# Optimization experiments

Measured on AMD Instinct MI355X. Metric: run time of the kernel, lower is better.

Reference implementation:

```python
import jax, jax.numpy as jnp
import numpy as np

H = 16          # num_heads
MAX_SCALE_MUL = float(np.log(100.0))
EPS = 1e-12     # F.normalize eps


def setup_inputs() -> dict:
    key = jax.random.key(0)
    ks = jax.random.split(key, 8)
    B, L, C = 8, 1024, 1024
    x = jax.random.normal(ks[0], (B, L, C), dtype=jnp.float32)
    attn_bias = jax.random.normal(ks[1], (1, H, L, L), dtype=jnp.float32) * 0.1
    w_qkv = jax.random.normal(ks[2], (3 * C, C), dtype=jnp.float32) * (C ** -0.5)
    q_bias = jnp.zeros((C,), dtype=jnp.float32)
    v_bias = jnp.zeros((C,), dtype=jnp.float32)
    scale_mul = jnp.full((1, H, 1, 1), np.log(4.0), dtype=jnp.float32)
    w_proj = jax.random.normal(ks[3], (C, C), dtype=jnp.float32) * (C ** -0.5)
    b_proj = jnp.zeros((C,), dtype=jnp.float32)
    return dict(x=x, attn_bias=attn_bias, w_qkv=w_qkv, q_bias=q_bias,
                v_bias=v_bias, scale_mul=scale_mul, w_proj=w_proj, b_proj=b_proj)


def _l2norm(t):
    # matches F.normalize(dim=-1): t / max(||t||_2, eps)
    n = jnp.sqrt(jnp.sum(t * t, axis=-1, keepdims=True))
    return t / jnp.maximum(n, EPS)


def reference(x, attn_bias, w_qkv, q_bias, v_bias, scale_mul, w_proj, b_proj):
    B, L, C = x.shape
    D = C // H
    bias = jnp.concatenate([q_bias, jnp.zeros_like(q_bias), v_bias])
    qkv = x @ w_qkv.T + bias                      # [B,L,3C]
    qkv = qkv.reshape(B, L, 3, H, D).transpose(2, 0, 3, 1, 4)  # [3,B,H,L,D]
    q, k, v = qkv[0], qkv[1], qkv[2]
    sm = jnp.exp(jnp.minimum(scale_mul, MAX_SCALE_MUL))        # [1,H,1,1]
    q = _l2norm(q) * sm
    k = _l2norm(k)
    attn = jnp.einsum('bhld,bhmd->bhlm', q, k) + attn_bias     # scale == 1
    attn = jax.nn.softmax(attn, axis=-1)
    out = jnp.einsum('bhlm,bhmd->bhld', attn, v)               # [B,H,L,D]
    out = out.transpose(0, 2, 1, 3).reshape(B, L, C)
    return out @ w_proj.T + b_proj
```

## Files before the change

### kernel.cpp

```cpp
#include <hip/hip_runtime.h>


#define LN100 4.6051701859880914f

typedef __attribute__((ext_vector_type(8))) short short8;
typedef __attribute__((ext_vector_type(4))) float f32x4;

#define MFMA_BF16(a, b, c) __builtin_amdgcn_mfma_f32_16x16x32_bf16(a, b, c, 0, 0, 0)

__device__ __forceinline__ unsigned short f2bf(float f) {
  unsigned u = __float_as_uint(f);
  u += 0x7fffu + ((u >> 16) & 1u);
  return (unsigned short)(u >> 16);
}
__device__ __forceinline__ float bf2f(unsigned short h) {
  return __uint_as_float(((unsigned)h) << 16);
}

__device__ __forceinline__ float bias_sel0(const float* qb, const float* vb, int col) {
  if (col < 1024) return qb[col];
  if (col < 2048) return 0.0f;
  return vb[col - 2048];
}

#define G2L16(gp, lp) __builtin_amdgcn_global_load_lds( \
    (const __attribute__((address_space(1))) void*)(gp), \
    (__attribute__((address_space(3))) void*)(lp), 16, 0, 0)

__global__ __launch_bounds__(256)
void split_f32_bf16(const float* __restrict__ in, unsigned short* __restrict__ hi,
                    unsigned short* __restrict__ lo, int n4)
{
  int i = blockIdx.x * blockDim.x + threadIdx.x;
  if (i >= n4) return;
  float4 v = ((const float4*)in)[i];
  ushort4 h, l;
  h.x = f2bf(v.x); l.x = f2bf(v.x - bf2f(h.x));
  h.y = f2bf(v.y); l.y = f2bf(v.y - bf2f(h.y));
  h.z = f2bf(v.z); l.z = f2bf(v.z - bf2f(h.z));
  h.w = f2bf(v.w); l.w = f2bf(v.w - bf2f(h.w));
  ((ushort4*)hi)[i] = h;
  ((ushort4*)lo)[i] = l;
}

template <int MODE>
__global__ __launch_bounds__(256)
void gemm_nt_split(const unsigned short* __restrict__ Ah, const unsigned short* __restrict__ Al,
                   const unsigned short* __restrict__ Wh, const unsigned short* __restrict__ Wl,
                   const float* __restrict__ b0, const float* __restrict__ b1,
                   float* __restrict__ C, int M, int N, int K)
{
  __shared__ unsigned short sA[128 * 64];
  __shared__ unsigned short sW[128 * 64];

  const int tid  = threadIdx.x;
  const int lane = tid & 63;
  const int l15  = lane & 15, lg = lane >> 4;
  const int w    = tid >> 6;
  const int wr   = (w >> 1) << 6;
  const int wc   = (w & 1) << 6;
  const int m0   = blockIdx.y << 7;
  const int n0   = blockIdx.x << 7;

  f32x4 acc[4][4];
  #pragma unroll
  for (int i = 0; i < 4; ++i)
    #pragma unroll
    for (int j = 0; j < 4; ++j)
      acc[i][j] = (f32x4){0.f, 0.f, 0.f, 0.f};

  for (int k0 = 0; k0 < K; k0 += 32) {
    __syncthreads();
    #pragma unroll
    for (int u = 0; u < 4; ++u) {
      int idx = (u << 8) + tid;
      int row = idx >> 3;
      int c   = idx & 7;
      int s   = c ^ (row & 7);
      size_t rbA = (size_t)(m0 + row) * K + k0;
      size_t rbW = (size_t)(n0 + row) * K + k0;
      const unsigned short* srcA = (s < 4) ? (Ah + rbA + (s << 3))
                                           : (Al + rbA + ((s - 4) << 3));
      const unsigned short* srcW = (s < 4) ? (Wh + rbW + (s << 3))
                                           : (Wl + rbW + ((s - 4) << 3));
      G2L16(srcA, sA + (idx << 3));
      G2L16(srcW, sW + (idx << 3));
    }
    __syncthreads();

    short8 ah[4], al[4];
    #pragma unroll
    for (int i = 0; i < 4; ++i) {
      int row = wr + (i << 4) + l15;
      ah[i] = *(const short8*)(sA + (row << 6) + ((lg       ^ (row & 7)) << 3));
      al[i] = *(const short8*)(sA + (row << 6) + (((4 + lg) ^ (row & 7)) << 3));
    }
    #pragma unroll
    for (int j = 0; j < 4; ++j) {
      int row = wc + (j << 4) + l15;
      short8 wh = *(const short8*)(sW + (row << 6) + ((lg       ^ (row & 7)) << 3));
      short8 wl = *(const short8*)(sW + (row << 6) + (((4 + lg) ^ (row & 7)) << 3));
      #pragma unroll
      for (int i = 0; i < 4; ++i) {
        acc[i][j] = MFMA_BF16(ah[i], wh, acc[i][j]);
        acc[i][j] = MFMA_BF16(ah[i], wl, acc[i][j]);
        acc[i][j] = MFMA_BF16(al[i], wh, acc[i][j]);
      }
    }
  }

  #pragma unroll
  for (int j = 0; j < 4; ++j) {
    int col = n0 + wc + (j << 4) + l15;
    float bb = (MODE == 0) ? bias_sel0(b0, b1, col) : b0[col];
    #pragma unroll
    for (int i = 0; i < 4; ++i) {
      int rbase = m0 + wr + (i << 4) + (lg << 2);
      #pragma unroll
      for (int r = 0; r < 4; ++r)
        C[(size_t)(rbase + r) * N + col] = acc[i][j][r] + bb;
    }
  }
}

__global__ __launch_bounds__(256)
void qk_norm_split(const float* __restrict__ qkv, const float* __restrict__ scale_mul,
                   unsigned short* __restrict__ qk_h, unsigned short* __restrict__ qk_l)
{
  int wave = (blockIdx.x << 2) + (threadIdx.x >> 6);
  int lane = threadIdx.x & 63;
  int h  = wave & 15;
  int bl = wave >> 4;
  size_t base = (size_t)bl * 3072 + (h << 6) + lane;
  float q = qkv[base];
  float k = qkv[base + 1024];
  float sq = q * q, sk = k * k;
  #pragma unroll
  for (int off = 32; off; off >>= 1) {
    sq += __shfl_xor(sq, off);
    sk += __shfl_xor(sk, off);
  }
  float sm = __expf(fminf(scale_mul[h], LN100));
  q = q / fmaxf(sqrtf(sq), 1e-12f) * sm;
  k = k / fmaxf(sqrtf(sk), 1e-12f);
  size_t ob = (size_t)bl * 2048 + (h << 6) + lane;
  unsigned short qh = f2bf(q);
  qk_h[ob] = qh;          qk_l[ob] = f2bf(q - bf2f(qh));
  unsigned short kh = f2bf(k);
  qk_h[ob + 1024] = kh;   qk_l[ob + 1024] = f2bf(k - bf2f(kh));
}

__global__ __launch_bounds__(256)
void v_split_t(const float* __restrict__ qkv, unsigned short* __restrict__ vth,
               unsigned short* __restrict__ vtl)
{
  __shared__ unsigned short Th[64][136];
  __shared__ unsigned short Tl[64][136];
  const int tid = threadIdx.x;
  const int kc = blockIdx.x & 7;
  const int h  = (blockIdx.x >> 3) & 15;
  const int b  = blockIdx.x >> 7;
  const int kv0 = kc << 7;

  #pragma unroll
  for (int u = 0; u < 8; ++u) {
    int idx = (u << 8) + tid;
    int kv  = idx >> 4;
    int d4  = (idx & 15) << 2;
    float4 v = *(const float4*)(qkv + (size_t)((b << 10) + kv0 + kv) * 3072
                                    + 2048 + (h << 6) + d4);
    float e[4] = {v.x, v.y, v.z, v.w};
    #pragma unroll
    for (int j = 0; j < 4; ++j) {
      unsigned short hb = f2bf(e[j]);
      Th[d4 + j][kv] = hb;
      Tl[d4 + j][kv] = f2bf(e[j] - bf2f(hb));
    }
  }
  __syncthreads();

  const size_t ob = ((size_t)((b << 4) + h) << 6) * 1024;
  #pragma unroll
  for (int u = 0; u < 4; ++u) {
    int idx = (u << 8) + tid;
    int d  = idx >> 4;
    int cc = idx & 15;
    short8 hv = *(const short8*)(&Th[d][cc << 3]);
    short8 lv = *(const short8*)(&Tl[d][cc << 3]);
    size_t go = ob + (size_t)d * 1024 + kv0 + (cc << 3);
    *(short8*)(vth + go) = hv;
    *(short8*)(vtl + go) = lv;
  }
}

__global__ __launch_bounds__(256)
void attn_mfma(const unsigned short* __restrict__ qk_h, const unsigned short* __restrict__ qk_l,
               const unsigned short* __restrict__ vth, const unsigned short* __restrict__ vtl,
               const float* __restrict__ bias,
               unsigned short* __restrict__ oh, unsigned short* __restrict__ ol)
{
  __shared__ unsigned short sKh[4096], sKl[4096];
  __shared__ unsigned short sVh[4096], sVl[4096];
  __shared__ unsigned short sPh[4096], sPl[4096];

  const int tid  = threadIdx.x;
  const int lane = tid & 63;
  const int l15  = lane & 15, lg = lane >> 4;
  const int w    = tid >> 6;
  const int qt = blockIdx.x & 15;
  const int h  = (blockIdx.x >> 4) & 15;
  const int b  = blockIdx.x >> 8;
  const int q0 = qt << 6;

  short8 qh[2], qlo[2];
  {
    size_t rb = ((size_t)((b << 10) + q0 + (w << 4) + l15)) * 2048 + (h << 6) + (lg << 3);
    qh[0]  = *(const short8*)(qk_h + rb);
    qh[1]  = *(const short8*)(qk_h + rb + 32);
    qlo[0] = *(const short8*)(qk_l + rb);
    qlo[1] = *(const short8*)(qk_l + rb + 32);
  }

  f32x4 ao[4];
  #pragma unroll
  for (int j = 0; j < 4; ++j) ao[j] = (f32x4){0.f, 0.f, 0.f, 0.f};
  float mr[4], lr[4];
  #pragma unroll
  for (int r = 0; r < 4; ++r) { mr[r] = -3.0e38f; lr[r] = 0.0f; }

  const unsigned short* kh_base = qk_h + 1024 + (h << 6);
  const unsigned short* kl_base = qk_l + 1024 + (h << 6);
  const size_t vbase = ((size_t)((b << 4) + h)) * 65536;

  for (int kv0 = 0; kv0 < 1024; kv0 += 64) {
    __syncthreads();
    #pragma unroll
    for (int u = 0; u < 2; ++u) {
      int idx = (u << 8) + tid;
      int r = idx >> 3, c = idx & 7;
      int s = c ^ (r & 7);
      size_t krow = (size_t)((b << 10) + kv0 + r) * 2048 + (s << 3);
      size_t vrow = vbase + (size_t)r * 1024 + kv0 + (s << 3);
      G2L16(kh_base + krow, sKh + (idx << 3));
      G2L16(kl_base + krow, sKl + (idx << 3));
      G2L16(vth + vrow,     sVh + (idx << 3));
      G2L16(vtl + vrow,     sVl + (idx << 3));
    }
    __syncthreads();

    f32x4 sv[4];
    #pragma unroll
    for (int j = 0; j < 4; ++j) {
      f32x4 a = (f32x4){0.f, 0.f, 0.f, 0.f};
      #pragma unroll
      for (int ks = 0; ks < 2; ++ks) {
        int row = (j << 4) + l15;
        int c   = (lg + (ks << 2)) ^ (row & 7);
        short8 kh = *(const short8*)(sKh + (row << 6) + (c << 3));
        short8 kl = *(const short8*)(sKl + (row << 6) + (c << 3));
        a = MFMA_BF16(qh[ks], kh, a);
        a = MFMA_BF16(qh[ks], kl, a);
        a = MFMA_BF16(qlo[ks], kh, a);
      }
      sv[j] = a;
    }

    float p[4][4], alpha[4];
    #pragma unroll
    for (int r = 0; r < 4; ++r) {
      int qrow = q0 + (w << 4) + (lg << 2) + r;
      const float* bp = bias + ((size_t)h << 20) + (size_t)qrow * 1024 + kv0 + l15;
      float s0 = sv[0][r] + bp[0];
      float s1 = sv[1][r] + bp[16];
      float s2 = sv[2][r] + bp[32];
      float s3 = sv[3][r] + bp[48];
      float mx = fmaxf(fmaxf(s0, s1), fmaxf(s2, s3));
      #pragma unroll
      for (int o = 1; o < 16; o <<= 1) mx = fmaxf(mx, __shfl_xor(mx, o));
      float mn = fmaxf(mr[r], mx);
      alpha[r] = __expf(mr[r] - mn);
      p[r][0] = __expf(s0 - mn); p[r][1] = __expf(s1 - mn);
      p[r][2] = __expf(s2 - mn); p[r][3] = __expf(s3 - mn);
      float rs = p[r][0] + p[r][1] + p[r][2] + p[r][3];
      #pragma unroll
      for (int o = 1; o < 16; o <<= 1) rs += __shfl_xor(rs, o);
      lr[r] = lr[r] * alpha[r] + rs;
      mr[r] = mn;
    }

    #pragma unroll
    for (int jd = 0; jd < 4; ++jd)
      #pragma unroll
      for (int r = 0; r < 4; ++r)
        ao[jd][r] *= alpha[r];

    #pragma unroll
    for (int r = 0; r < 4; ++r) {
      int q2 = (w << 4) + (lg << 2) + r;
      #pragma unroll
      for (int j = 0; j < 4; ++j) {
        unsigned short hb = f2bf(p[r][j]);
        unsigned short lb = f2bf(p[r][j] - bf2f(hb));
        int c = ((j << 1) + (l15 >> 3)) ^ (q2 & 7);
        int e = (q2 << 6) + (c << 3) + (l15 & 7);
        sPh[e] = hb;
        sPl[e] = lb;
      }
    }

    #pragma unroll
    for (int ks = 0; ks < 2; ++ks) {
      int prow = (w << 4) + l15;
      int pc   = (lg + (ks << 2)) ^ (prow & 7);
      short8 ph = *(const short8*)(sPh + (prow << 6) + (pc << 3));
      short8 pl = *(const short8*)(sPl + (prow << 6) + (pc << 3));
      #pragma unroll
      for (int jd = 0; jd < 4; ++jd) {
        int vrow = (jd << 4) + l15;
        int vc   = (lg + (ks << 2)) ^ (vrow & 7);
        short8 vh = *(const short8*)(sVh + (vrow << 6) + (vc << 3));
        short8 vl = *(const short8*)(sVl + (vrow << 6) + (vc << 3));
        ao[jd] = MFMA_BF16(ph, vh, ao[jd]);
        ao[jd] = MFMA_BF16(ph, vl, ao[jd]);
        ao[jd] = MFMA_BF16(pl, vh, ao[jd]);
      }
    }
  }

  #pragma unroll
  for (int r = 0; r < 4; ++r) {
    float inv = 1.0f / lr[r];
    size_t orow = ((size_t)((b << 10) + q0 + (w << 4) + (lg << 2) + r)) * 1024
                + (h << 6) + l15;
    #pragma unroll
    for (int jd = 0; jd < 4; ++jd) {
      float v = ao[jd][r] * inv;
      unsigned short hb = f2bf(v);
      oh[orow + (jd << 4)] = hb;
      ol[orow + (jd << 4)] = f2bf(v - bf2f(hb));
    }
  }
}

template <int MODE>
__global__ __launch_bounds__(256)
void gemm_nt(const float* __restrict__ A, const float* __restrict__ Bw,
             const float* __restrict__ b0, const float* __restrict__ b1,
             float* __restrict__ C, int M, int N, int K)
{
  __shared__ float As[32][132];
  __shared__ float Bs[32][132];
  const int tid = threadIdx.x;
  const int tx = tid & 15, ty = tid >> 4;
  const int m0 = blockIdx.y << 7;
  const int n0 = blockIdx.x << 7;

  float acc[8][8];
  #pragma unroll
  for (int i = 0; i < 8; ++i)
    #pragma unroll
    for (int j = 0; j < 8; ++j) acc[i][j] = 0.0f;

  for (int k0 = 0; k0 < K; k0 += 32) {
    #pragma unroll
    for (int u = 0; u < 4; ++u) {
      int f   = tid + (u << 8);
      int row = f >> 3;
      int kk  = (f & 7) << 2;
      float4 av = *(const float4*)(A  + (size_t)(m0 + row) * K + k0 + kk);
      As[kk + 0][row] = av.x; As[kk + 1][row] = av.y;
      As[kk + 2][row] = av.z; As[kk + 3][row] = av.w;
      float4 bv = *(const float4*)(Bw + (size_t)(n0 + row) * K + k0 + kk);
      Bs[kk + 0][row] = bv.x; Bs[kk + 1][row] = bv.y;
      Bs[kk + 2][row] = bv.z; Bs[kk + 3][row] = bv.w;
    }
    __syncthreads();
    #pragma unroll
    for (int kk = 0; kk < 32; ++kk) {
      float a[8], b[8];
      *(float4*)(a)     = *(const float4*)(&As[kk][(ty << 3)]);
      *(float4*)(a + 4) = *(const float4*)(&As[kk][(ty << 3) + 4]);
      *(float4*)(b)     = *(const float4*)(&Bs[kk][(tx << 3)]);
      *(float4*)(b + 4) = *(const float4*)(&Bs[kk][(tx << 3) + 4]);
      #pragma unroll
      for (int i = 0; i < 8; ++i)
        #pragma unroll
        for (int j = 0; j < 8; ++j)
          acc[i][j] = fmaf(a[i], b[j], acc[i][j]);
    }
    __syncthreads();
  }

  #pragma unroll
  for (int i = 0; i < 8; ++i) {
    int row = m0 + (ty << 3) + i;
    #pragma unroll
    for (int j4 = 0; j4 < 2; ++j4) {
      int col = n0 + (tx << 3) + (j4 << 2);
      float4 r;
      float bb[4];
      #pragma unroll
      for (int j = 0; j < 4; ++j)
        bb[j] = (MODE == 0) ? bias_sel0(b0, b1, col + j) : b0[col + j];
      r.x = acc[i][j4 * 4 + 0] + bb[0];
      r.y = acc[i][j4 * 4 + 1] + bb[1];
      r.z = acc[i][j4 * 4 + 2] + bb[2];
      r.w = acc[i][j4 * 4 + 3] + bb[3];
      *(float4*)(C + (size_t)row * N + col) = r;
    }
  }
}

__global__ __launch_bounds__(256)
void qk_norm(float* __restrict__ qkv, const float* __restrict__ scale_mul)
{
  int wave = (blockIdx.x << 2) + (threadIdx.x >> 6);
  int lane = threadIdx.x & 63;
  int h  = wave & 15;
  int bl = wave >> 4;
  size_t base = (size_t)bl * 3072 + (h << 6) + lane;
  float q = qkv[base];
  float k = qkv[base + 1024];
  float sq = q * q, sk = k * k;
  #pragma unroll
  for (int off = 32; off; off >>= 1) {
    sq += __shfl_xor(sq, off);
    sk += __shfl_xor(sk, off);
  }
  float sm = __expf(fminf(scale_mul[h], LN100));
  q = q / fmaxf(sqrtf(sq), 1e-12f) * sm;
  k = k / fmaxf(sqrtf(sk), 1e-12f);
  qkv[base]        = q;
  qkv[base + 1024] = k;
}

#define SW(r, c4) ((((c4) ^ ((r) >> 2)) & 15) << 2)

template <int OUTMODE>
__global__ __launch_bounds__(256)
void attn_fwd(const float* __restrict__ qkv, const float* __restrict__ bias,
              float* __restrict__ aout,
              unsigned short* __restrict__ ah, unsigned short* __restrict__ al)
{
  __shared__ float Qs[64][64];
  __shared__ float Ks[64][64];
  __shared__ float Vs[64][64];
  __shared__ float Ps[64][64];

  const int tid = threadIdx.x;
  const int tx = tid & 15, ty = tid >> 4;
  const int qt = blockIdx.x & 15;
  const int h  = (blockIdx.x >> 4) & 15;
  const int b  = blockIdx.x >> 8;
  const int q0 = qt << 6;

  #pragma unroll
  for (int u = 0; u < 4; ++u) {
    int f = tid + (u << 8);
    int r = f >> 4, c4 = f & 15;
    float4 v = *(const float4*)(qkv + (size_t)(b * 1024 + q0 + r) * 3072 + (h << 6) + (c4 << 2));
    *(float4*)(&Qs[r][SW(r, c4)]) = v;
  }

  float o[4][4];
  float mr[4], lr[4];
  #pragma unroll
  for (int i = 0; i < 4; ++i) {
    mr[i] = -3.0e38f; lr[i] = 0.0f;
    #pragma unroll
    for (int j = 0; j < 4; ++j) o[i][j] = 0.0f;
  }

  for (int kv0 = 0; kv0 < 1024; kv0 += 64) {
    __syncthreads();
    #pragma unroll
    for (int u = 0; u < 4; ++u) {
      int f = tid + (u << 8);
      int r = f >> 4, c4 = f & 15;
      size_t gb = (size_t)(b * 1024 + kv0 + r) * 3072 + (h << 6) + (c4 << 2);
      *(float4*)(&Ks[r][SW(r, c4)]) = *(const float4*)(qkv + gb + 1024);
      *(float4*)(&Vs[r][SW(r, c4)]) = *(const float4*)(qkv + gb + 2048);
    }
    __syncthreads();

    float s[4][4];
    #pragma unroll
    for (int i = 0; i < 4; ++i)
      #pragma unroll
      for (int j = 0; j < 4; ++j) s[i][j] = 0.0f;

    #pragma unroll 4
    for (int d4 = 0; d4 < 16; ++d4) {
      float4 qv[4], kv[4];
      #pragma unroll
      for (int i = 0; i < 4; ++i)
        qv[i] = *(const float4*)(&Qs[(ty << 2) + i][SW((ty << 2) + i, d4)]);
      #pragma unroll
      for (int j = 0; j < 4; ++j)
        kv[j] = *(const float4*)(&Ks[(tx << 2) + j][SW((tx << 2) + j, d4)]);
      #pragma unroll
      for (int i = 0; i < 4; ++i)
        #pragma unroll
        for (int j = 0; j < 4; ++j)
          s[i][j] += qv[i].x * kv[j].x + qv[i].y * kv[j].y +
                     qv[i].z * kv[j].z + qv[i].w * kv[j].w;
    }

    float p[4][4];
    #pragma unroll
    for (int i = 0; i < 4; ++i) {
      float4 bv = *(const float4*)(bias + (size_t)((h << 10) + q0 + (ty << 2) + i) * 1024
                                        + kv0 + (tx << 2));
      s[i][0] += bv.x; s[i][1] += bv.y; s[i][2] += bv.z; s[i][3] += bv.w;
      float mx = fmaxf(fmaxf(s[i][0], s[i][1]), fmaxf(s[i][2], s[i][3]));
      #pragma unroll
      for (int off = 1; off < 16; off <<= 1) mx = fmaxf(mx, __shfl_xor(mx, off));
      float mn = fmaxf(mr[i], mx);
      float alp = __expf(mr[i] - mn);
      float rs = 0.0f;
      #pragma unroll
      for (int j = 0; j < 4; ++j) { p[i][j] = __expf(s[i][j] - mn); rs += p[i][j]; }
      #pragma unroll
      for (int off = 1; off < 16; off <<= 1) rs += __shfl_xor(rs, off);
      lr[i] = lr[i] * alp + rs;
      mr[i] = mn;
      #pragma unroll
      for (int j = 0; j < 4; ++j) o[i][j] *= alp;
    }

    #pragma unroll
    for (int jj = 0; jj < 4; ++jj)
      #pragma unroll
      for (int i = 0; i < 4; ++i)
        Ps[(tx << 2) + jj][SW((tx << 2) + jj, ty) + i] = p[i][jj];
    __syncthreads();

    #pragma unroll 8
    for (int j = 0; j < 64; ++j) {
      float4 pv = *(const float4*)(&Ps[j][SW(j, ty)]);
      float4 vv = *(const float4*)(&Vs[j][SW(j, tx)]);
      o[0][0] += pv.x * vv.x; o[0][1] += pv.x * vv.y; o[0][2] += pv.x * vv.z; o[0][3] += pv.x * vv.w;
      o[1][0] += pv.y * vv.x; o[1][1] += pv.y * vv.y; o[1][2] += pv.y * vv.z; o[1][3] += pv.y * vv.w;
      o[2][0] += pv.z * vv.x; o[2][1] += pv.z * vv.y; o[2][2] += pv.z * vv.z; o[2][3] += pv.z * vv.w;
      o[3][0] += pv.w * vv.x; o[3][1] += pv.w * vv.y; o[3][2] += pv.w * vv.z; o[3][3] += pv.w * vv.w;
    }
  }

  #pragma unroll
  for (int i = 0; i < 4; ++i) {
    float inv = 1.0f / lr[i];
    float v0 = o[i][0] * inv, v1 = o[i][1] * inv, v2 = o[i][2] * inv, v3 = o[i][3] * inv;
    if (OUTMODE == 0) {
      float4 r; r.x = v0; r.y = v1; r.z = v2; r.w = v3;
      *(float4*)(aout + (size_t)(b * 1024 + q0 + (ty << 2) + i) * 1024 + (h << 6) + (tx << 2)) = r;
    } else {
      ushort4 hh, ll;
      hh.x = f2bf(v0); ll.x = f2bf(v0 - bf2f(hh.x));
      hh.y = f2bf(v1); ll.y = f2bf(v1 - bf2f(hh.y));
      hh.z = f2bf(v2); ll.z = f2bf(v2 - bf2f(hh.z));
      hh.w = f2bf(v3); ll.w = f2bf(v3 - bf2f(hh.w));
      size_t idx = (size_t)(b * 1024 + q0 + (ty << 2) + i) * 256 + (h << 4) + tx;
      ((ushort4*)ah)[idx] = hh;
      ((ushort4*)al)[idx] = ll;
    }
  }
}

extern "C" void kernel_launch(void* const* d_in, const int* in_sizes, int n_in,
                              void* d_out, int out_size, void* d_ws, size_t ws_size,
                              hipStream_t stream) {
  const float* x         = (const float*)d_in[0];
  const float* attn_bias = (const float*)d_in[1];
  const float* w_qkv     = (const float*)d_in[2];
  const float* q_bias    = (const float*)d_in[3];
  const float* v_bias    = (const float*)d_in[4];
  const float* scale_mul = (const float*)d_in[5];
  const float* w_proj    = (const float*)d_in[6];
  const float* b_proj    = (const float*)d_in[7];
  float* out = (float*)d_out;

  const size_t MiB = 1024 * 1024;
  char* ws = (char*)d_ws;
  dim3 blk(256);

  if (ws_size >= 240 * MiB) {
    float*          qkv = (float*)ws;
    unsigned short* xh  = (unsigned short*)(ws + 96  * MiB);
    unsigned short* xl  = (unsigned short*)(ws + 112 * MiB);
    unsigned short* qkh = (unsigned short*)(ws + 128 * MiB);
    unsigned short* qkl = (unsigned short*)(ws + 160 * MiB);
    unsigned short* vth = (unsigned short*)(ws + 192 * MiB);
    unsigned short* vtl = (unsigned short*)(ws + 208 * MiB);
    unsigned short* wqh = (unsigned short*)(ws + 224 * MiB);
    unsigned short* wql = (unsigned short*)(ws + 230 * MiB);
    unsigned short* wph = (unsigned short*)(ws + 236 * MiB);
    unsigned short* wpl = (unsigned short*)(ws + 238 * MiB);

    split_f32_bf16<<<dim3(8192), blk, 0, stream>>>(x,      xh,  xl,  2097152);
    split_f32_bf16<<<dim3(3072), blk, 0, stream>>>(w_qkv,  wqh, wql, 786432);
    split_f32_bf16<<<dim3(1024), blk, 0, stream>>>(w_proj, wph, wpl, 262144);

    gemm_nt_split<0><<<dim3(24, 64), blk, 0, stream>>>(xh, xl, wqh, wql,
        q_bias, v_bias, qkv, 8192, 3072, 1024);
    qk_norm_split<<<dim3(32768), blk, 0, stream>>>(qkv, scale_mul, qkh, qkl);
    v_split_t<<<dim3(1024), blk, 0, stream>>>(qkv, vth, vtl);
    attn_mfma<<<dim3(2048), blk, 0, stream>>>(qkh, qkl, vth, vtl, attn_bias, xh, xl);
    gemm_nt_split<1><<<dim3(8, 64), blk, 0, stream>>>(xh, xl, wph, wpl,
        b_proj, nullptr, out, 8192, 1024, 1024);
  } else if (ws_size >= 144 * MiB) {
    float*          qkv = (float*)ws;
    unsigned short* xh  = (unsigned short*)(ws + 96  * MiB);
    unsigned short* xl  = (unsigned short*)(ws + 112 * MiB);
    unsigned short* wqh = (unsigned short*)(ws + 128 * MiB);
    unsigned short* wql = (unsigned short*)(ws + 134 * MiB);
    unsigned short* wph = (unsigned short*)(ws + 140 * MiB);
    unsigned short* wpl = (unsigned short*)(ws + 142 * MiB);

    split_f32_bf16<<<dim3(8192), blk, 0, stream>>>(x,      xh,  xl,  2097152);
    split_f32_bf16<<<dim3(3072), blk, 0, stream>>>(w_qkv,  wqh, wql, 786432);
    split_f32_bf16<<<dim3(1024), blk, 0, stream>>>(w_proj, wph, wpl, 262144);

    gemm_nt_split<0><<<dim3(24, 64), blk, 0, stream>>>(xh, xl, wqh, wql,
        q_bias, v_bias, qkv, 8192, 3072, 1024);
    qk_norm<<<dim3(32768), blk, 0, stream>>>(qkv, scale_mul);
    attn_fwd<1><<<dim3(2048), blk, 0, stream>>>(qkv, attn_bias, nullptr, xh, xl);
    gemm_nt_split<1><<<dim3(8, 64), blk, 0, stream>>>(xh, xl, wph, wpl,
        b_proj, nullptr, out, 8192, 1024, 1024);
  } else {
    float* qkv = (float*)ws;
    float* att = qkv + (size_t)8192 * 3072;
    gemm_nt<0><<<dim3(24, 64), blk, 0, stream>>>(x, w_qkv, q_bias, v_bias, qkv, 8192, 3072, 1024);
    qk_norm<<<dim3(32768), blk, 0, stream>>>(qkv, scale_mul);
    attn_fwd<0><<<dim3(2048), blk, 0, stream>>>(qkv, attn_bias, att, nullptr, nullptr);
    gemm_nt<1><<<dim3(8, 64), blk, 0, stream>>>(att, w_proj, b_proj, nullptr, out, 8192, 1024, 1024);
  }
}
```

Baseline: 648.9 us.

## Fuse V split-transpose into QKV GEMM epilogue and double attention query tile

The QKV GEMM epilogue now writes the V columns straight into the transposed bf16 hi/lo V buffers, so the separate v_split_t kernel and its extra read of the fp32 V slice are gone. The attention kernel now handles 128 query rows per block (two 16-row fragments per wave), which halves the grid and reuses each K/V tile loaded into LDS across twice as many queries. Bias loads are hoisted ahead of the barrier to overlap with the LDS fills. In exchange, registers and LDS use go up, and the transposed V stores are 8-byte scattered writes that may coalesce poorly.

```diff
diff --git a/kernel.cpp b/kernel.cpp
--- a/kernel.cpp
+++ b/kernel.cpp
@@ -48,7 +48,9 @@
 void gemm_nt_split(const unsigned short* __restrict__ Ah, const unsigned short* __restrict__ Al,
                    const unsigned short* __restrict__ Wh, const unsigned short* __restrict__ Wl,
                    const float* __restrict__ b0, const float* __restrict__ b1,
-                   float* __restrict__ C, int M, int N, int K)
+                   float* __restrict__ C,
+                   unsigned short* __restrict__ vth, unsigned short* __restrict__ vtl,
+                   int M, int N, int K)
 {
   __shared__ unsigned short sA[128 * 64];
   __shared__ unsigned short sW[128 * 64];
@@ -109,16 +111,45 @@
     }
   }
 
-  #pragma unroll
-  for (int j = 0; j < 4; ++j) {
-    int col = n0 + wc + (j << 4) + l15;
-    float bb = (MODE == 0) ? bias_sel0(b0, b1, col) : b0[col];
-    #pragma unroll
-    for (int i = 0; i < 4; ++i) {
-      int rbase = m0 + wr + (i << 4) + (lg << 2);
-      #pragma unroll
-      for (int r = 0; r < 4; ++r)
-        C[(size_t)(rbase + r) * N + col] = acc[i][j][r] + bb;
+  if (MODE == 0 && n0 >= 2048) {
+    #pragma unroll
+    for (int j = 0; j < 4; ++j) {
+      int col = n0 + wc + (j << 4) + l15;
+      int d   = col - 2048;
+      int hh  = d >> 6, dd = d & 63;
+      float bb = b1[d];
+      #pragma unroll
+      for (int i = 0; i < 4; ++i) {
+        int row  = m0 + wr + (i << 4) + (lg << 2);
+        int bidx = row >> 10;
+        int l    = row & 1023;
+        size_t obase = ((((size_t)bidx << 4) + hh) << 6) + dd;
+        obase = obase * 1024 + l;
+        ushort4 hv, lv;
+        float v0 = acc[i][j][0] + bb;
+        float v1 = acc[i][j][1] + bb;
+        float v2 = acc[i][j][2] + bb;
+        float v3 = acc[i][j][3] + bb;
+        hv.x = f2bf(v0); lv.x = f2bf(v0 - bf2f(hv.x));
+        hv.y = f2bf(v1); lv.y = f2bf(v1 - bf2f(hv.y));
+        hv.z = f2bf(v2); lv.z = f2bf(v2 - bf2f(hv.z));
+        hv.w = f2bf(v3); lv.w = f2bf(v3 - bf2f(hv.w));
+        *(ushort4*)(vth + obase) = hv;
+        *(ushort4*)(vtl + obase) = lv;
+      }
+    }
+  } else {
+    #pragma unroll
+    for (int j = 0; j < 4; ++j) {
+      int col = n0 + wc + (j << 4) + l15;
+      float bb = (MODE == 1) ? b0[col] : bias_sel0(b0, b1, col);
+      #pragma unroll
+      for (int i = 0; i < 4; ++i) {
+        int rbase = m0 + wr + (i << 4) + (lg << 2);
+        #pragma unroll
+        for (int r = 0; r < 4; ++r)
+          C[(size_t)(rbase + r) * N + col] = acc[i][j][r] + bb;
+      }
     }
   }
 }
@@ -150,50 +181,7 @@
   qk_h[ob + 1024] = kh;   qk_l[ob + 1024] = f2bf(k - bf2f(kh));
 }
 
-__global__ __launch_bounds__(256)
-void v_split_t(const float* __restrict__ qkv, unsigned short* __restrict__ vth,
-               unsigned short* __restrict__ vtl)
-{
-  __shared__ unsigned short Th[64][136];
-  __shared__ unsigned short Tl[64][136];
-  const int tid = threadIdx.x;
-  const int kc = blockIdx.x & 7;
-  const int h  = (blockIdx.x >> 3) & 15;
-  const int b  = blockIdx.x >> 7;
-  const int kv0 = kc << 7;
-
-  #pragma unroll
-  for (int u = 0; u < 8; ++u) {
-    int idx = (u << 8) + tid;
-    int kv  = idx >> 4;
-    int d4  = (idx & 15) << 2;
-    float4 v = *(const float4*)(qkv + (size_t)((b << 10) + kv0 + kv) * 3072
-                                    + 2048 + (h << 6) + d4);
-    float e[4] = {v.x, v.y, v.z, v.w};
-    #pragma unroll
-    for (int j = 0; j < 4; ++j) {
-      unsigned short hb = f2bf(e[j]);
-      Th[d4 + j][kv] = hb;
-      Tl[d4 + j][kv] = f2bf(e[j] - bf2f(hb));
-    }
-  }
-  __syncthreads();
-
-  const size_t ob = ((size_t)((b << 4) + h) << 6) * 1024;
-  #pragma unroll
-  for (int u = 0; u < 4; ++u) {
-    int idx = (u << 8) + tid;
-    int d  = idx >> 4;
-    int cc = idx & 15;
-    short8 hv = *(const short8*)(&Th[d][cc << 3]);
-    short8 lv = *(const short8*)(&Tl[d][cc << 3]);
-    size_t go = ob + (size_t)d * 1024 + kv0 + (cc << 3);
-    *(short8*)(vth + go) = hv;
-    *(short8*)(vtl + go) = lv;
-  }
-}
-
-__global__ __launch_bounds__(256)
+__global__ __launch_bounds__(256, 2)
 void attn_mfma(const unsigned short* __restrict__ qk_h, const unsigned short* __restrict__ qk_l,
                const unsigned short* __restrict__ vth, const unsigned short* __restrict__ vtl,
                const float* __restrict__ bias,
@@ -201,32 +189,37 @@
 {
   __shared__ unsigned short sKh[4096], sKl[4096];
   __shared__ unsigned short sVh[4096], sVl[4096];
-  __shared__ unsigned short sPh[4096], sPl[4096];
+  __shared__ unsigned short sPh[8192], sPl[8192];
 
   const int tid  = threadIdx.x;
   const int lane = tid & 63;
   const int l15  = lane & 15, lg = lane >> 4;
   const int w    = tid >> 6;
-  const int qt = blockIdx.x & 15;
-  const int h  = (blockIdx.x >> 4) & 15;
-  const int b  = blockIdx.x >> 8;
-  const int q0 = qt << 6;
-
-  short8 qh[2], qlo[2];
-  {
-    size_t rb = ((size_t)((b << 10) + q0 + (w << 4) + l15)) * 2048 + (h << 6) + (lg << 3);
-    qh[0]  = *(const short8*)(qk_h + rb);
-    qh[1]  = *(const short8*)(qk_h + rb + 32);
-    qlo[0] = *(const short8*)(qk_l + rb);
-    qlo[1] = *(const short8*)(qk_l + rb + 32);
-  }
-
-  f32x4 ao[4];
-  #pragma unroll
-  for (int j = 0; j < 4; ++j) ao[j] = (f32x4){0.f, 0.f, 0.f, 0.f};
-  float mr[4], lr[4];
-  #pragma unroll
-  for (int r = 0; r < 4; ++r) { mr[r] = -3.0e38f; lr[r] = 0.0f; }
+  const int qt = blockIdx.x & 7;
+  const int h  = (blockIdx.x >> 3) & 15;
+  const int b  = blockIdx.x >> 7;
+  const int q0 = qt << 7;
+
+  short8 qh[2][2], qlo[2][2];
+  #pragma unroll
+  for (int qf = 0; qf < 2; ++qf) {
+    size_t rb = ((size_t)((b << 10) + q0 + (w << 5) + (qf << 4) + l15)) * 2048
+              + (h << 6) + (lg << 3);
+    qh[qf][0]  = *(const short8*)(qk_h + rb);
+    qh[qf][1]  = *(const short8*)(qk_h + rb + 32);
+    qlo[qf][0] = *(const short8*)(qk_l + rb);
+    qlo[qf][1] = *(const short8*)(qk_l + rb + 32);
+  }
+
+  f32x4 ao[2][4];
+  float mr[2][4], lr[2][4];
+  #pragma unroll
+  for (int qf = 0; qf < 2; ++qf) {
+    #pragma unroll
+    for (int j = 0; j < 4; ++j) ao[qf][j] = (f32x4){0.f, 0.f, 0.f, 0.f};
+    #pragma unroll
+    for (int r = 0; r < 4; ++r) { mr[qf][r] = -3.0e38f; lr[qf][r] = 0.0f; }
+  }
 
   const unsigned short* kh_base = qk_h + 1024 + (h << 6);
   const unsigned short* kl_base = qk_l + 1024 + (h << 6);
@@ -246,100 +239,123 @@
       G2L16(vth + vrow,     sVh + (idx << 3));
       G2L16(vtl + vrow,     sVl + (idx << 3));
     }
-    __syncthreads();
-
-    f32x4 sv[4];
+    float bb[2][4][4];
+    #pragma unroll
+    for (int qf = 0; qf < 2; ++qf)
+      #pragma unroll
+      for (int r = 0; r < 4; ++r) {
+        int qrow = q0 + (w << 5) + (qf << 4) + (lg << 2) + r;
+        const float* bp = bias + ((size_t)h << 20) + (size_t)qrow * 1024 + kv0 + l15;
+        #pragma unroll
+        for (int j = 0; j < 4; ++j) bb[qf][r][j] = bp[j << 4];
+      }
+    __syncthreads();
+
+    f32x4 sv[2][4];
     #pragma unroll
     for (int j = 0; j < 4; ++j) {
-      f32x4 a = (f32x4){0.f, 0.f, 0.f, 0.f};
+      f32x4 a0 = (f32x4){0.f, 0.f, 0.f, 0.f};
+      f32x4 a1 = (f32x4){0.f, 0.f, 0.f, 0.f};
       #pragma unroll
       for (int ks = 0; ks < 2; ++ks) {
         int row = (j << 4) + l15;
         int c   = (lg + (ks << 2)) ^ (row & 7);
         short8 kh = *(const short8*)(sKh + (row << 6) + (c << 3));
         short8 kl = *(const short8*)(sKl + (row << 6) + (c << 3));
-        a = MFMA_BF16(qh[ks], kh, a);
-        a = MFMA_BF16(qh[ks], kl, a);
-        a = MFMA_BF16(qlo[ks], kh, a);
-      }
-      sv[j] = a;
-    }
-
-    float p[4][4], alpha[4];
-    #pragma unroll
-    for (int r = 0; r < 4; ++r) {
-      int qrow = q0 + (w << 4) + (lg << 2) + r;
-      const float* bp = bias + ((size_t)h << 20) + (size_t)qrow * 1024 + kv0 + l15;
-      float s0 = sv[0][r] + bp[0];
-      float s1 = sv[1][r] + bp[16];
-      float s2 = sv[2][r] + bp[32];
-      float s3 = sv[3][r] + bp[48];
-      float mx = fmaxf(fmaxf(s0, s1), fmaxf(s2, s3));
-      #pragma unroll
-      for (int o = 1; o < 16; o <<= 1) mx = fmaxf(mx, __shfl_xor(mx, o));
-      float mn = fmaxf(mr[r], mx);
-      alpha[r] = __expf(mr[r] - mn);
-      p[r][0] = __expf(s0 - mn); p[r][1] = __expf(s1 - mn);
-      p[r][2] = __expf(s2 - mn); p[r][3] = __expf(s3 - mn);
-      float rs = p[r][0] + p[r][1] + p[r][2] + p[r][3];
-      #pragma unroll
-      for (int o = 1; o < 16; o <<= 1) rs += __shfl_xor(rs, o);
-      lr[r] = lr[r] * alpha[r] + rs;
-      mr[r] = mn;
-    }
-
-    #pragma unroll
-    for (int jd = 0; jd < 4; ++jd)
-      #pragma unroll
-      for (int r = 0; r < 4; ++r)
-        ao[jd][r] *= alpha[r];
-
-    #pragma unroll
-    for (int r = 0; r < 4; ++r) {
-      int q2 = (w << 4) + (lg << 2) + r;
-      #pragma unroll
-      for (int j = 0; j < 4; ++j) {
-        unsigned short hb = f2bf(p[r][j]);
-        unsigned short lb = f2bf(p[r][j] - bf2f(hb));
-        int c = ((j << 1) + (l15 >> 3)) ^ (q2 & 7);
-        int e = (q2 << 6) + (c << 3) + (l15 & 7);
-        sPh[e] = hb;
-        sPl[e] = lb;
+        a0 = MFMA_BF16(qh[0][ks], kh, a0);
+        a0 = MFMA_BF16(qh[0][ks], kl, a0);
+        a0 = MFMA_BF16(qlo[0][ks], kh, a0);
+        a1 = MFMA_BF16(qh[1][ks], kh, a1);
+        a1 = MFMA_BF16(qh[1][ks], kl, a1);
+        a1 = MFMA_BF16(qlo[1][ks], kh, a1);
+      }
+      sv[0][j] = a0;
+      sv[1][j] = a1;
+    }
+
+    #pragma unroll
+    for (int qf = 0; qf < 2; ++qf) {
+      float p[4][4], alpha[4];
+      #pragma unroll
+      for (int r = 0; r < 4; ++r) {
+        float s0 = sv[qf][0][r] + bb[qf][r][0];
+        float s1 = sv[qf][1][r] + bb[qf][r][1];
+        float s2 = sv[qf][2][r] + bb[qf][r][2];
+        float s3 = sv[qf][3][r] + bb[qf][r][3];
+        float mx = fmaxf(fmaxf(s0, s1), fmaxf(s2, s3));
+        #pragma unroll
+        for (int o = 1; o < 16; o <<= 1) mx = fmaxf(mx, __shfl_xor(mx, o));
+        float mn = fmaxf(mr[qf][r], mx);
+        alpha[r] = __expf(mr[qf][r] - mn);
+        p[r][0] = __expf(s0 - mn); p[r][1] = __expf(s1 - mn);
+        p[r][2] = __expf(s2 - mn); p[r][3] = __expf(s3 - mn);
+        float rs = p[r][0] + p[r][1] + p[r][2] + p[r][3];
+        #pragma unroll
+        for (int o = 1; o < 16; o <<= 1) rs += __shfl_xor(rs, o);
+        lr[qf][r] = lr[qf][r] * alpha[r] + rs;
+        mr[qf][r] = mn;
+      }
+      #pragma unroll
+      for (int jd = 0; jd < 4; ++jd)
+        #pragma unroll
+        for (int r = 0; r < 4; ++r)
+          ao[qf][jd][r] *= alpha[r];
+      #pragma unroll
+      for (int r = 0; r < 4; ++r) {
+        int q2 = (w << 5) + (qf << 4) + (lg << 2) + r;
+        #pragma unroll
+        for (int j = 0; j < 4; ++j) {
+          unsigned short hb = f2bf(p[r][j]);
+          unsigned short lb = f2bf(p[r][j] - bf2f(hb));
+          int c = ((j << 1) + (l15 >> 3)) ^ (q2 & 7);
+          int e = (q2 << 6) + (c << 3) + (l15 & 7);
+          sPh[e] = hb;
+          sPl[e] = lb;
+        }
       }
     }
 
     #pragma unroll
     for (int ks = 0; ks < 2; ++ks) {
-      int prow = (w << 4) + l15;
-      int pc   = (lg + (ks << 2)) ^ (prow & 7);
-      short8 ph = *(const short8*)(sPh + (prow << 6) + (pc << 3));
-      short8 pl = *(const short8*)(sPl + (prow << 6) + (pc << 3));
+      short8 ph[2], pl[2];
+      #pragma unroll
+      for (int qf = 0; qf < 2; ++qf) {
+        int prow = (w << 5) + (qf << 4) + l15;
+        int pc   = (lg + (ks << 2)) ^ (prow & 7);
+        ph[qf] = *(const short8*)(sPh + (prow << 6) + (pc << 3));
+        pl[qf] = *(const short8*)(sPl + (prow << 6) + (pc << 3));
+      }
       #pragma unroll
       for (int jd = 0; jd < 4; ++jd) {
         int vrow = (jd << 4) + l15;
         int vc   = (lg + (ks << 2)) ^ (vrow & 7);
         short8 vh = *(const short8*)(sVh + (vrow << 6) + (vc << 3));
         short8 vl = *(const short8*)(sVl + (vrow << 6) + (vc << 3));
-        ao[jd] = MFMA_BF16(ph, vh, ao[jd]);
-        ao[jd] = MFMA_BF16(ph, vl, ao[jd]);
-        ao[jd] = MFMA_BF16(pl, vh, ao[jd]);
-      }
-    }
-  }
-
-  #pragma unroll
-  for (int r = 0; r < 4; ++r) {
-    float inv = 1.0f / lr[r];
-    size_t orow = ((size_t)((b << 10) + q0 + (w << 4) + (lg << 2) + r)) * 1024
-                + (h << 6) + l15;
-    #pragma unroll
-    for (int jd = 0; jd < 4; ++jd) {
-      float v = ao[jd][r] * inv;
-      unsigned short hb = f2bf(v);
-      oh[orow + (jd << 4)] = hb;
-      ol[orow + (jd << 4)] = f2bf(v - bf2f(hb));
-    }
-  }
+        #pragma unroll
+        for (int qf = 0; qf < 2; ++qf) {
+          ao[qf][jd] = MFMA_BF16(ph[qf], vh, ao[qf][jd]);
+          ao[qf][jd] = MFMA_BF16(ph[qf], vl, ao[qf][jd]);
+          ao[qf][jd] = MFMA_BF16(pl[qf], vh, ao[qf][jd]);
+        }
+      }
+    }
+  }
+
+  #pragma unroll
+  for (int qf = 0; qf < 2; ++qf)
+    #pragma unroll
+    for (int r = 0; r < 4; ++r) {
+      float inv = 1.0f / lr[qf][r];
+      size_t orow = ((size_t)((b << 10) + q0 + (w << 5) + (qf << 4) + (lg << 2) + r)) * 1024
+                  + (h << 6) + l15;
+      #pragma unroll
+      for (int jd = 0; jd < 4; ++jd) {
+        float v = ao[qf][jd][r] * inv;
+        unsigned short hb = f2bf(v);
+        oh[orow + (jd << 4)] = hb;
+        ol[orow + (jd << 4)] = f2bf(v - bf2f(hb));
+      }
+    }
 }
 
 template <int MODE>
@@ -601,12 +617,11 @@
     split_f32_bf16<<<dim3(1024), blk, 0, stream>>>(w_proj, wph, wpl, 262144);
 
     gemm_nt_split<0><<<dim3(24, 64), blk, 0, stream>>>(xh, xl, wqh, wql,
-        q_bias, v_bias, qkv, 8192, 3072, 1024);
+        q_bias, v_bias, qkv, vth, vtl, 8192, 3072, 1024);
     qk_norm_split<<<dim3(32768), blk, 0, stream>>>(qkv, scale_mul, qkh, qkl);
-    v_split_t<<<dim3(1024), blk, 0, stream>>>(qkv, vth, vtl);
-    attn_mfma<<<dim3(2048), blk, 0, stream>>>(qkh, qkl, vth, vtl, attn_bias, xh, xl);
+    attn_mfma<<<dim3(1024), blk, 0, stream>>>(qkh, qkl, vth, vtl, attn_bias, xh, xl);
     gemm_nt_split<1><<<dim3(8, 64), blk, 0, stream>>>(xh, xl, wph, wpl,
-        b_proj, nullptr, out, 8192, 1024, 1024);
+        b_proj, nullptr, out, nullptr, nullptr, 8192, 1024, 1024);
   } else if (ws_size >= 144 * MiB) {
     float*          qkv = (float*)ws;
     unsigned short* xh  = (unsigned short*)(ws + 96  * MiB);
@@ -620,12 +635,12 @@
     split_f32_bf16<<<dim3(3072), blk, 0, stream>>>(w_qkv,  wqh, wql, 786432);
     split_f32_bf16<<<dim3(1024), blk, 0, stream>>>(w_proj, wph, wpl, 262144);
 
-    gemm_nt_split<0><<<dim3(24, 64), blk, 0, stream>>>(xh, xl, wqh, wql,
-        q_bias, v_bias, qkv, 8192, 3072, 1024);
+    gemm_nt_split<2><<<dim3(24, 64), blk, 0, stream>>>(xh, xl, wqh, wql,
+        q_bias, v_bias, qkv, nullptr, nullptr, 8192, 3072, 1024);
     qk_norm<<<dim3(32768), blk, 0, stream>>>(qkv, scale_mul);
     attn_fwd<1><<<dim3(2048), blk, 0, stream>>>(qkv, attn_bias, nullptr, xh, xl);
     gemm_nt_split<1><<<dim3(8, 64), blk, 0, stream>>>(xh, xl, wph, wpl,
-        b_proj, nullptr, out, 8192, 1024, 1024);
+        b_proj, nullptr, out, nullptr, nullptr, 8192, 1024, 1024);
   } else {
     float* qkv = (float*)ws;
     float* att = qkv + (size_t)8192 * 3072;
```

After: 602.3 us. 7.2% less time.
